# Performance work log

Measured on AMD Instinct MI355X. Metric: run time of the kernel, lower is better.

## Reference

```python
import jax, jax.numpy as jnp
import numpy as np

B, N, C, F, O = 32, 2048, 8, 128, 128


def setup_inputs() -> dict:
    key = jax.random.key(0)
    k1, k2, k3, k4, k5, k6 = jax.random.split(key, 6)
    nodes = jax.random.normal(k1, (B, N, F), dtype=jnp.float32)
    children = jax.random.randint(k2, (B, N, C), 0, N, dtype=jnp.int32)
    w_t = jax.random.normal(k3, (F, O), dtype=jnp.float32) * 0.05
    w_l = jax.random.normal(k4, (F, O), dtype=jnp.float32) * 0.05
    w_r = jax.random.normal(k5, (F, O), dtype=jnp.float32) * 0.05
    b = jax.random.normal(k6, (O,), dtype=jnp.float32) * 0.05
    return {"nodes": nodes, "children": children, "w_t": w_t, "w_l": w_l, "w_r": w_r, "b": b}


def reference(nodes, children, w_t, w_l, w_r, b):
    Bb, Nn, Ff = nodes.shape
    Cc = children.shape[2]
    dt = nodes.dtype

    # --- children tensor: index 0 maps to zero vector ---
    lookup = jnp.concatenate([jnp.zeros((Bb, 1, Ff), dt), nodes[:, 1:, :]], axis=1)
    batch_idx = jnp.arange(Bb)[:, None, None]
    child_vecs = lookup[batch_idx, children]                      # [B,N,C,F]
    tree = jnp.concatenate([nodes[:, :, None, :], child_vecs], axis=2)  # [B,N,C+1,F]

    # --- coefficients ---
    ch_f = children.astype(dt)
    c_t = jnp.broadcast_to(
        jnp.concatenate([jnp.ones((1, 1, 1), dt), jnp.zeros((1, 1, Cc), dt)], axis=2),
        (Bb, Nn, Cc + 1))                                          # [B,N,C+1]
    num_sib = jnp.count_nonzero(children, axis=2, keepdims=True).astype(dt)  # [B,N,1]
    mask = jnp.concatenate(
        [jnp.zeros((Bb, Nn, 1), dt), jnp.minimum(ch_f, 1.0)], axis=2)        # [B,N,C+1]
    child_indices = jnp.arange(-1.0, Cc, 1.0, dtype=dt)[None, None, :] * mask
    singles = jnp.concatenate(
        [jnp.zeros((Bb, Nn, 1), dt),
         jnp.full((Bb, Nn, 1), 0.5, dt),
         jnp.zeros((Bb, Nn, Cc - 1), dt)], axis=2)
    is_single = num_sib == 1.0
    denom = jnp.where(is_single, 1.0, num_sib - 1.0)  # safe divide, matches tf.where select
    c_r = jnp.where(is_single, singles, (1.0 - c_t) * (child_indices / denom))
    c_l = (1.0 - c_t) * (1.0 - c_r) * mask
    coef = jnp.stack([c_t, c_r, c_l], axis=3)                      # [B,N,C+1,3]

    # --- weighted aggregation + small GEMM ---
    agg = jnp.einsum('bncf,bnck->bnkf', tree, coef)                # [B,N,3,F]
    w = jnp.stack([w_t, w_r, w_l], axis=0)                         # [3,F,O]
    out = jnp.einsum('bnkf,kfo->bno', agg, w)
    return jax.nn.relu(out + b)
```

## Files before the change

kernel.cpp:

```cpp
#include <hip/hip_runtime.h>

typedef unsigned short ushort_t;
typedef __attribute__((ext_vector_type(8))) short short8;
typedef __attribute__((ext_vector_type(4))) short short4v;
typedef __attribute__((ext_vector_type(4))) float float4v;

#define Bn 32
#define Nn 2048
#define Cn 8
#define Fn 128
#define On 128
#define Kn 384
#define MT 32
#define LDSK 392

__device__ __forceinline__ ushort_t f2bf(float x) {
  unsigned u = __float_as_uint(x);
  u += 0x7fffu + ((u >> 16) & 1u);
  return (ushort_t)(u >> 16);
}

__global__ void prep_w_kernel(const float* __restrict__ w_t,
                              const float* __restrict__ w_l,
                              const float* __restrict__ w_r,
                              ushort_t* __restrict__ wsw) {
  int t = blockIdx.x * blockDim.x + threadIdx.x;
  if (t >= 6144) return;
  int lane = t & 63;
  int r = t >> 6;
  int ks = r % 12;
  int q = r / 12;
  int ct = q & 1;
  int w = q >> 1;
  int col = w * 32 + ct * 16 + (lane & 15);
  int kbase = ((lane >> 4) * 8) + ks * 32;
  ushort_t* dst = wsw + (size_t)t * 8;
#pragma unroll
  for (int j = 0; j < 8; ++j) {
    int k = kbase + j;
    const float* src = (k < Fn) ? w_t : (k < 2 * Fn) ? w_r : w_l;
    int f = k & (Fn - 1);
    dst[j] = f2bf(src[f * On + col]);
  }
}

__global__ __launch_bounds__(256)
void tree_conv_kernel(const float* __restrict__ nodes,
                      const int* __restrict__ children,
                      const ushort_t* __restrict__ wsw,
                      const float* __restrict__ bias,
                      float* __restrict__ out) {
  __shared__ __align__(16) ushort_t agg[MT * LDSK];

  const int tid = threadIdx.x;

  const int sb = ((blockIdx.x & 7) << 8) | (blockIdx.x >> 3);

  {
    const int grp = tid >> 5;
    const int ln = tid & 31;

#pragma unroll
    for (int it = 0; it < 4; ++it) {
      const int row = it * 8 + grp;
      const int g = sb * MT + row;
      const int base_row = g & ~(Nn - 1);

      const int4* chv = (const int4*)(children + (size_t)g * Cn);
      int4 ca = chv[0], cb = chv[1];
      int idx[Cn] = {ca.x, ca.y, ca.z, ca.w, cb.x, cb.y, cb.z, cb.w};

      int ns = 0;
#pragma unroll
      for (int c = 0; c < Cn; ++c) ns += (idx[c] != 0);
      const float denom = (ns > 1) ? (float)(ns - 1) : 1.0f;

      float crv[Cn], clv[Cn];
#pragma unroll
      for (int c = 0; c < Cn; ++c) {
        float m = (idx[c] != 0) ? 1.0f : 0.0f;
        float cr0 = (ns == 1) ? ((c == 0) ? 0.5f : 0.0f) : ((float)c / denom);
        float cr = cr0 * m;
        crv[c] = cr;
        clv[c] = (1.0f - cr) * m;
        idx[c] &= (Nn - 1);
      }

      const float4v sv = *((const float4v*)(nodes + (size_t)g * Fn) + ln);

      float4v rr = {0.f, 0.f, 0.f, 0.f};
      float4v ll = {0.f, 0.f, 0.f, 0.f};
#pragma unroll
      for (int c = 0; c < Cn; ++c) {
        const float4v v =
            *((const float4v*)(nodes + (size_t)(base_row + idx[c]) * Fn) + ln);
        rr += crv[c] * v;
        ll += clv[c] * v;
      }

      ushort_t* arow = agg + row * LDSK;
      short4v ps = {(short)f2bf(sv.x), (short)f2bf(sv.y),
                    (short)f2bf(sv.z), (short)f2bf(sv.w)};
      short4v pr = {(short)f2bf(rr.x), (short)f2bf(rr.y),
                    (short)f2bf(rr.z), (short)f2bf(rr.w)};
      short4v pl = {(short)f2bf(ll.x), (short)f2bf(ll.y),
                    (short)f2bf(ll.z), (short)f2bf(ll.w)};
      *(short4v*)(arow + ln * 4) = ps;
      *(short4v*)(arow + Fn + ln * 4) = pr;
      *(short4v*)(arow + 2 * Fn + ln * 4) = pl;
    }
  }

  __syncthreads();

  const int lane = tid & 63;
  const int wave = tid >> 6;
  const int l15 = lane & 15;
  const int quad = lane >> 4;

#pragma unroll
  for (int ct = 0; ct < 2; ++ct) {
    const short8* bp = (const short8*)wsw + ((wave * 2 + ct) * 12) * 64 + lane;
    short8 bfrag[12];
#pragma unroll
    for (int ks = 0; ks < 12; ++ks) bfrag[ks] = bp[ks * 64];

    const int col = wave * 32 + ct * 16 + l15;
    const float bb = bias[col];

#pragma unroll
    for (int st = 0; st < 2; ++st) {
      const ushort_t* ar = agg + (st * 16 + l15) * LDSK + quad * 8;
      float4v acc = {0.f, 0.f, 0.f, 0.f};
#pragma unroll
      for (int ks = 0; ks < 12; ++ks) {
        short8 af = *(const short8*)(ar + ks * 32);
        acc = __builtin_amdgcn_mfma_f32_16x16x32_bf16(af, bfrag[ks], acc, 0, 0, 0);
      }
      const int grow0 = sb * MT + st * 16 + quad * 4;
#pragma unroll
      for (int r2 = 0; r2 < 4; ++r2) {
        out[(size_t)(grow0 + r2) * On + col] = fmaxf(acc[r2] + bb, 0.f);
      }
    }
  }
}

extern "C" void kernel_launch(void* const* d_in, const int* in_sizes, int n_in,
                              void* d_out, int out_size, void* d_ws, size_t ws_size,
                              hipStream_t stream) {
  const float* nodes = (const float*)d_in[0];
  const int* children = (const int*)d_in[1];
  const float* w_t = (const float*)d_in[2];
  const float* w_l = (const float*)d_in[3];
  const float* w_r = (const float*)d_in[4];
  const float* bias = (const float*)d_in[5];
  float* out = (float*)d_out;
  ushort_t* wsw = (ushort_t*)d_ws;

  prep_w_kernel<<<24, 256, 0, stream>>>(w_t, w_l, w_r, wsw);
  tree_conv_kernel<<<(Bn * Nn) / MT, 256, 0, stream>>>(nodes, children, wsw, bias, out);
}
```

Measured before the change: 122.9 us.

## Halve row tile and widen per-thread gather with packed FMA and bf16 truncation

The row tile per block drops from 32 to 16, so there are twice as many blocks. Each thread now aggregates 8 features of a single row in one pass instead of looping over four rows. Child accumulation uses packed float2 FMAs, the divide becomes a reciprocal, and fp32-to-bf16 conversion becomes a truncating byte permute with wider 16-byte LDS stores. The aim is more memory parallelism for the gather and fewer conversion instructions. In exchange, weight fragments are reloaded for every block, which doubles weight traffic. Truncation also loses round-to-nearest accuracy.

```diff
diff --git a/kernel.cpp b/kernel.cpp
--- a/kernel.cpp
+++ b/kernel.cpp
@@ -1,8 +1,10 @@
 #include <hip/hip_runtime.h>
 
 typedef unsigned short ushort_t;
+typedef unsigned int uint_t;
 typedef __attribute__((ext_vector_type(8))) short short8;
-typedef __attribute__((ext_vector_type(4))) short short4v;
+typedef __attribute__((ext_vector_type(4))) uint_t uint4v;
+typedef __attribute__((ext_vector_type(2))) float float2v;
 typedef __attribute__((ext_vector_type(4))) float float4v;
 
 #define Bn 32
@@ -10,14 +12,18 @@
 #define Cn 8
 #define Fn 128
 #define On 128
-#define Kn 384
-#define MT 32
+#define MT 16
 #define LDSK 392
 
 __device__ __forceinline__ ushort_t f2bf(float x) {
   unsigned u = __float_as_uint(x);
   u += 0x7fffu + ((u >> 16) & 1u);
   return (ushort_t)(u >> 16);
+}
+
+__device__ __forceinline__ uint_t pk2bf(float lo, float hi) {
+  return __builtin_amdgcn_perm(__float_as_uint(hi), __float_as_uint(lo),
+                               0x07060302u);
 }
 
 __global__ void prep_w_kernel(const float* __restrict__ w_t,
@@ -30,9 +36,7 @@
   int r = t >> 6;
   int ks = r % 12;
   int q = r / 12;
-  int ct = q & 1;
-  int w = q >> 1;
-  int col = w * 32 + ct * 16 + (lane & 15);
+  int col = q * 16 + (lane & 15);
   int kbase = ((lane >> 4) * 8) + ks * 32;
   ushort_t* dst = wsw + (size_t)t * 8;
 #pragma unroll
@@ -53,62 +57,68 @@
   __shared__ __align__(16) ushort_t agg[MT * LDSK];
 
   const int tid = threadIdx.x;
-
-  const int sb = ((blockIdx.x & 7) << 8) | (blockIdx.x >> 3);
+  const int sb = ((blockIdx.x & 7) << 9) | (blockIdx.x >> 3);
+  const int rb0 = sb * MT;
 
   {
-    const int grp = tid >> 5;
-    const int ln = tid & 31;
+    const int row = tid >> 4;
+    const int ln = tid & 15;
+    const int g = rb0 + row;
+    const int base_row = g & ~(Nn - 1);
+
+    const int4* chv = (const int4*)(children + (size_t)g * Cn);
+    int4 ca = chv[0], cb = chv[1];
+    int idx[Cn] = {ca.x, ca.y, ca.z, ca.w, cb.x, cb.y, cb.z, cb.w};
+
+    int ns = 0;
+#pragma unroll
+    for (int c = 0; c < Cn; ++c) ns += (idx[c] != 0);
+    const float rden = __builtin_amdgcn_rcpf((ns > 1) ? (float)(ns - 1) : 1.0f);
+    const bool single = (ns == 1);
+
+    float crv[Cn], clv[Cn];
+#pragma unroll
+    for (int c = 0; c < Cn; ++c) {
+      float m = (idx[c] != 0) ? 1.0f : 0.0f;
+      float cr0 = single ? ((c == 0) ? 0.5f : 0.0f) : ((float)c * rden);
+      float cr = cr0 * m;
+      crv[c] = cr;
+      clv[c] = (1.0f - cr) * m;
+      idx[c] &= (Nn - 1);
+    }
+
+    const float4v* sp = (const float4v*)(nodes + (size_t)g * Fn) + ln * 2;
+    const float4v s0 = sp[0], s1 = sp[1];
+
+    float2v rl[8];
+#pragma unroll
+    for (int e = 0; e < 8; ++e) rl[e] = (float2v){0.f, 0.f};
 
 #pragma unroll
-    for (int it = 0; it < 4; ++it) {
-      const int row = it * 8 + grp;
-      const int g = sb * MT + row;
-      const int base_row = g & ~(Nn - 1);
+    for (int c = 0; c < Cn; ++c) {
+      const float4v* cp =
+          (const float4v*)(nodes + (size_t)(base_row + idx[c]) * Fn) + ln * 2;
+      const float4v v0 = cp[0], v1 = cp[1];
+      const float2v cc = {crv[c], clv[c]};
+      rl[0] += (float2v){v0.x, v0.x} * cc;
+      rl[1] += (float2v){v0.y, v0.y} * cc;
+      rl[2] += (float2v){v0.z, v0.z} * cc;
+      rl[3] += (float2v){v0.w, v0.w} * cc;
+      rl[4] += (float2v){v1.x, v1.x} * cc;
+      rl[5] += (float2v){v1.y, v1.y} * cc;
+      rl[6] += (float2v){v1.z, v1.z} * cc;
+      rl[7] += (float2v){v1.w, v1.w} * cc;
+    }
 
-      const int4* chv = (const int4*)(children + (size_t)g * Cn);
-      int4 ca = chv[0], cb = chv[1];
-      int idx[Cn] = {ca.x, ca.y, ca.z, ca.w, cb.x, cb.y, cb.z, cb.w};
-
-      int ns = 0;
-#pragma unroll
-      for (int c = 0; c < Cn; ++c) ns += (idx[c] != 0);
-      const float denom = (ns > 1) ? (float)(ns - 1) : 1.0f;
-
-      float crv[Cn], clv[Cn];
-#pragma unroll
-      for (int c = 0; c < Cn; ++c) {
-        float m = (idx[c] != 0) ? 1.0f : 0.0f;
-        float cr0 = (ns == 1) ? ((c == 0) ? 0.5f : 0.0f) : ((float)c / denom);
-        float cr = cr0 * m;
-        crv[c] = cr;
-        clv[c] = (1.0f - cr) * m;
-        idx[c] &= (Nn - 1);
-      }
-
-      const float4v sv = *((const float4v*)(nodes + (size_t)g * Fn) + ln);
-
-      float4v rr = {0.f, 0.f, 0.f, 0.f};
-      float4v ll = {0.f, 0.f, 0.f, 0.f};
-#pragma unroll
-      for (int c = 0; c < Cn; ++c) {
-        const float4v v =
-            *((const float4v*)(nodes + (size_t)(base_row + idx[c]) * Fn) + ln);
-        rr += crv[c] * v;
-        ll += clv[c] * v;
-      }
-
-      ushort_t* arow = agg + row * LDSK;
-      short4v ps = {(short)f2bf(sv.x), (short)f2bf(sv.y),
-                    (short)f2bf(sv.z), (short)f2bf(sv.w)};
-      short4v pr = {(short)f2bf(rr.x), (short)f2bf(rr.y),
-                    (short)f2bf(rr.z), (short)f2bf(rr.w)};
-      short4v pl = {(short)f2bf(ll.x), (short)f2bf(ll.y),
-                    (short)f2bf(ll.z), (short)f2bf(ll.w)};
-      *(short4v*)(arow + ln * 4) = ps;
-      *(short4v*)(arow + Fn + ln * 4) = pr;
-      *(short4v*)(arow + 2 * Fn + ln * 4) = pl;
-    }
+    ushort_t* arow = agg + row * LDSK + ln * 8;
+    *(uint4v*)(arow) = (uint4v){pk2bf(s0.x, s0.y), pk2bf(s0.z, s0.w),
+                                pk2bf(s1.x, s1.y), pk2bf(s1.z, s1.w)};
+    *(uint4v*)(arow + Fn) =
+        (uint4v){pk2bf(rl[0].x, rl[1].x), pk2bf(rl[2].x, rl[3].x),
+                 pk2bf(rl[4].x, rl[5].x), pk2bf(rl[6].x, rl[7].x)};
+    *(uint4v*)(arow + 2 * Fn) =
+        (uint4v){pk2bf(rl[0].y, rl[1].y), pk2bf(rl[2].y, rl[3].y),
+                 pk2bf(rl[4].y, rl[5].y), pk2bf(rl[6].y, rl[7].y)};
   }
 
   __syncthreads();
@@ -117,32 +127,29 @@
   const int wave = tid >> 6;
   const int l15 = lane & 15;
   const int quad = lane >> 4;
+  const ushort_t* ar = agg + l15 * LDSK + quad * 8;
 
 #pragma unroll
   for (int ct = 0; ct < 2; ++ct) {
-    const short8* bp = (const short8*)wsw + ((wave * 2 + ct) * 12) * 64 + lane;
+    const int q = wave * 2 + ct;
     short8 bfrag[12];
 #pragma unroll
-    for (int ks = 0; ks < 12; ++ks) bfrag[ks] = bp[ks * 64];
+    for (int ks = 0; ks < 12; ++ks)
+      bfrag[ks] = ((const short8*)wsw)[(q * 12 + ks) * 64 + lane];
 
-    const int col = wave * 32 + ct * 16 + l15;
+    const int col = q * 16 + l15;
     const float bb = bias[col];
 
+    float4v acc = {0.f, 0.f, 0.f, 0.f};
 #pragma unroll
-    for (int st = 0; st < 2; ++st) {
-      const ushort_t* ar = agg + (st * 16 + l15) * LDSK + quad * 8;
-      float4v acc = {0.f, 0.f, 0.f, 0.f};
+    for (int ks = 0; ks < 12; ++ks) {
+      const short8 af = *(const short8*)(ar + ks * 32);
+      acc = __builtin_amdgcn_mfma_f32_16x16x32_bf16(af, bfrag[ks], acc, 0, 0, 0);
+    }
+    const int grow = rb0 + quad * 4;
 #pragma unroll
-      for (int ks = 0; ks < 12; ++ks) {
-        short8 af = *(const short8*)(ar + ks * 32);
-        acc = __builtin_amdgcn_mfma_f32_16x16x32_bf16(af, bfrag[ks], acc, 0, 0, 0);
-      }
-      const int grow0 = sb * MT + st * 16 + quad * 4;
-#pragma unroll
-      for (int r2 = 0; r2 < 4; ++r2) {
-        out[(size_t)(grow0 + r2) * On + col] = fmaxf(acc[r2] + bb, 0.f);
-      }
-    }
+    for (int r2 = 0; r2 < 4; ++r2)
+      out[(size_t)(grow + r2) * On + col] = fmaxf(acc[r2] + bb, 0.f);
   }
 }
 
@@ -159,5 +166,6 @@
   ushort_t* wsw = (ushort_t*)d_ws;
 
   prep_w_kernel<<<24, 256, 0, stream>>>(w_t, w_l, w_r, wsw);
-  tree_conv_kernel<<<(Bn * Nn) / MT, 256, 0, stream>>>(nodes, children, wsw, bias, out);
+  tree_conv_kernel<<<(Bn * Nn) / MT, 256, 0, stream>>>(nodes, children, wsw,
+                                                       bias, out);
 }
```

Result: faster. 118.3 us (-3.8%).
